# Performance work log

Hardware: AMD Instinct MI355X
Metric: run time of the kernel (lower is better)

## Reference

```python
import jax, jax.numpy as jnp
import numpy as np

CROSSOVER_MAGNITUDE = 0.3
MUTATION_FACTOR = 0.3

B, A, H = 16, 512, 8  # batch, activation_size (== dim_emb), n_head


def setup_inputs() -> dict:
    key = jax.random.key(0)
    ks = jax.random.split(key, 11)
    d = A
    s = 0.02  # small init scale for weights
    return {
        "Q": jax.random.normal(ks[0], (B, A, A), jnp.float32),
        "K": jax.random.normal(ks[1], (B, A, A), jnp.float32),
        "V": jax.random.normal(ks[2], (B, A), jnp.float32),
        "WQ_w": jax.random.normal(ks[3], (d, d), jnp.float32) * s,
        "WQ_b": jax.random.normal(ks[4], (d,), jnp.float32) * s,
        "WK_w": jax.random.normal(ks[5], (d, d), jnp.float32) * s,
        "WK_b": jax.random.normal(ks[6], (d,), jnp.float32) * s,
        "WV_w": jax.random.normal(ks[7], (d, d), jnp.float32) * s,
        "WV_b": jax.random.normal(ks[8], (d,), jnp.float32) * s,
        "WO_w": jax.random.normal(ks[9], (d, d * H), jnp.float32) * s,
        "WO_b": jax.random.normal(ks[10], (d,), jnp.float32) * s,
    }


def _attention_core(Qp, Kp, Vp, WO_w, WO_b):
    # Qp, Kp: (B, A, A) projected; identical across heads in the original
    # (heads are copies stacked before shared Linear), so compute once
    # and broadcast. Vp: (B, A).
    rkey = jax.random.key(42)
    kp, km, kr1, kr2 = jax.random.split(rkey, 4)

    am0 = jnp.einsum('bji,bjk->bik', Qp, Kp) / jnp.sqrt(jnp.float32(8.0))
    am = jnp.broadcast_to(am0[:, None], (B, H, A, A))  # (B,H,A,A)

    def mutate(a):
        # elementwise multiply by U(1-mf, 1+mf) noise
        m = jax.random.uniform(km, a.shape, jnp.float32,
                               1.0 - MUTATION_FACTOR, 1.0 + MUTATION_FACTOR)
        return a * m

    def crossover(a):
        # swap the tail segments [c:] of two random rows per (batch, head)
        c = A - int(A * CROSSOVER_MAGNITUDE)
        r1 = jax.random.randint(kr1, (B, H), 0, A)
        r2 = jax.random.randint(kr2, (B, H), 0, A)
        bi = jnp.arange(B)[:, None]
        hi = jnp.arange(H)[None, :]
        tails = a[..., c:]                     # (B,H,A,A-c)
        t1 = tails[bi, hi, r1]                 # (B,H,A-c)
        t2 = tails[bi, hi, r2]
        tails = tails.at[bi, hi, r1].set(t2).at[bi, hi, r2].set(t1)
        return jnp.concatenate([a[..., :c], tails], axis=-1)

    p = jax.random.uniform(kp, ())
    am = jax.lax.cond(p <= 0.6, mutate, crossover, am)

    attn = jax.nn.softmax(am, axis=-1)               # (B,H,A,A)
    out = jnp.einsum('bhij,bj->bhi', attn, Vp)       # attn @ V[...,None] squeezed
    out = out.reshape(B, H * A)
    return out @ WO_w.T + WO_b                       # (B, A)


def reference(Q, K, V, WQ_w, WQ_b, WK_w, WK_b, WV_w, WV_b, WO_w, WO_b):
    Qp = Q @ WQ_w.T + WQ_b   # (B,A,A), same for every head
    Kp = K @ WK_w.T + WK_b
    Vp = V @ WV_w.T + WV_b   # (B,A)
    return _attention_core(Qp, Kp, Vp, WO_w, WO_b)
```

## Files before the change

kernel.cpp:

```cpp
#include <hip/hip_runtime.h>
#include <stdint.h>
#include <string.h>

#define B_ 16
#define A_ 512
#define H_ 8
#define C_CROSS 359
#define LDSTRIDE 40

typedef short short8 __attribute__((ext_vector_type(8)));
typedef float floatx4 __attribute__((ext_vector_type(4)));

__host__ __device__ __forceinline__ uint32_t rotl32(uint32_t x, int r) {
#ifdef __HIP_DEVICE_COMPILE__
  return __builtin_amdgcn_alignbit(x, x, 32 - r);
#else
  return (x << r) | (x >> (32 - r));
#endif
}

__host__ __device__ __forceinline__ void tf2x32(uint32_t k0, uint32_t k1,
                                                uint32_t x0, uint32_t x1,
                                                uint32_t& o0, uint32_t& o1) {
  uint32_t ks2 = k0 ^ k1 ^ 0x1BD11BDAu;
  x0 += k0; x1 += k1;
#define TFR(r) { x0 += x1; x1 = rotl32(x1, r); x1 ^= x0; }
  TFR(13) TFR(15) TFR(26) TFR(6)   x0 += k1;  x1 += ks2 + 1u;
  TFR(17) TFR(29) TFR(16) TFR(24)  x0 += ks2; x1 += k0 + 2u;
  TFR(13) TFR(15) TFR(26) TFR(6)   x0 += k0;  x1 += k1 + 3u;
  TFR(17) TFR(29) TFR(16) TFR(24)  x0 += k1;  x1 += ks2 + 4u;
  TFR(13) TFR(15) TFR(26) TFR(6)   x0 += ks2; x1 += k0 + 5u;
#undef TFR
  o0 = x0; o1 = x1;
}

__host__ __device__ __forceinline__ float bits2u01(uint32_t bits) {
  uint32_t v = (bits >> 9) | 0x3f800000u;
  float f;
#ifdef __HIP_DEVICE_COMPILE__
  f = __uint_as_float(v);
#else
  memcpy(&f, &v, 4);
#endif
  return f - 1.0f;
}

__device__ __forceinline__ void tsplit(float x, short& h, short& l) {
  uint32_t u = __float_as_uint(x);
  float hf = __uint_as_float(u & 0xffff0000u);
  h = (short)(u >> 16);
  l = (short)(__float_as_uint(x - hf) >> 16);
}

__device__ __forceinline__ void tsplit8(const float4& v0, const float4& v1,
                                        short8& h, short8& l) {
  float xs[8] = {v0.x, v0.y, v0.z, v0.w, v1.x, v1.y, v1.z, v1.w};
#pragma unroll
  for (int j = 0; j < 8; ++j) {
    short hh, ll;
    tsplit(xs[j], hh, ll);
    h[j] = hh; l[j] = ll;
  }
}

__global__ __launch_bounds__(256, 2) void lin_mfma2(
    const float* __restrict__ Xq, const float* __restrict__ Wq,
    const float* __restrict__ bq, ushort* __restrict__ QptH, ushort* __restrict__ QptL,
    const float* __restrict__ Xk, const float* __restrict__ Wk,
    const float* __restrict__ bk, ushort* __restrict__ KptH, ushort* __restrict__ KptL) {
  int bid = blockIdx.x;
  int z = bid >> 8;
  int rem = bid & 255;
  int ti = rem >> 2, tn = rem & 3;
  const float* X = z ? Xk : Xq;
  const float* W = z ? Wk : Wq;
  const float* bias = z ? bk : bq;
  ushort* OH = z ? KptH : QptH;
  ushort* OL = z ? KptL : QptL;

  __shared__ __align__(16) char smem[40960];
  ushort (*Ah)[LDSTRIDE] = (ushort(*)[LDSTRIDE])(smem);
  ushort (*Al)[LDSTRIDE] = (ushort(*)[LDSTRIDE])(smem + 10240);
  ushort (*Bh)[LDSTRIDE] = (ushort(*)[LDSTRIDE])(smem + 20480);
  ushort (*Bl)[LDSTRIDE] = (ushort(*)[LDSTRIDE])(smem + 30720);
  uint32_t (*cs)[132] = (uint32_t(*)[132])(smem);

  int tid = threadIdx.x;
  int w = tid >> 6, lane = tid & 63, quad = lane >> 4, l16 = lane & 15;
  int wm = (w >> 1) * 64, wn = (w & 1) * 64;
  int m0 = ti * 128;
  int n0 = tn * 128;

  float bv[4];
#pragma unroll
  for (int nt = 0; nt < 4; ++nt) bv[nt] = bias[n0 + wn + nt * 16 + l16];

  const float* pX[2];
  const float* pW[2];
  int mW[2], kgW[2];
#pragma unroll
  for (int g = 0; g < 2; ++g) {
    int gid = g * 256 + tid;
    int m = gid >> 2, kg = gid & 3;
    mW[g] = m; kgW[g] = kg;
    pX[g] = X + (size_t)(m0 + m) * 512 + kg * 8;
    pW[g] = W + (size_t)(n0 + m) * 512 + kg * 8;
  }

  float4 ra[2][2], rb[2][2];
#pragma unroll
  for (int g = 0; g < 2; ++g) {
    ra[g][0] = *(const float4*)(pX[g]);
    ra[g][1] = *(const float4*)(pX[g] + 4);
    rb[g][0] = *(const float4*)(pW[g]);
    rb[g][1] = *(const float4*)(pW[g] + 4);
  }

  floatx4 acc[4][4] = {};

  for (int k0 = 0; k0 < 512; k0 += 32) {
    __syncthreads();
#pragma unroll
    for (int g = 0; g < 2; ++g) {
      short8 h8, l8;
      tsplit8(ra[g][0], ra[g][1], h8, l8);
      *(short8*)&Ah[mW[g]][kgW[g] * 8] = h8;
      *(short8*)&Al[mW[g]][kgW[g] * 8] = l8;
      tsplit8(rb[g][0], rb[g][1], h8, l8);
      *(short8*)&Bh[mW[g]][kgW[g] * 8] = h8;
      *(short8*)&Bl[mW[g]][kgW[g] * 8] = l8;
    }
    __syncthreads();
    if (k0 < 480) {
      int kn = k0 + 32;
#pragma unroll
      for (int g = 0; g < 2; ++g) {
        ra[g][0] = *(const float4*)(pX[g] + kn);
        ra[g][1] = *(const float4*)(pX[g] + kn + 4);
        rb[g][0] = *(const float4*)(pW[g] + kn);
        rb[g][1] = *(const float4*)(pW[g] + kn + 4);
      }
    }
    short8 fAh[4], fAl[4], fBh[4], fBl[4];
#pragma unroll
    for (int t4 = 0; t4 < 4; ++t4) {
      int ma = wm + t4 * 16 + l16;
      int nb = wn + t4 * 16 + l16;
      fAh[t4] = *(const short8*)&Ah[ma][quad * 8];
      fAl[t4] = *(const short8*)&Al[ma][quad * 8];
      fBh[t4] = *(const short8*)&Bh[nb][quad * 8];
      fBl[t4] = *(const short8*)&Bl[nb][quad * 8];
    }
#pragma unroll
    for (int mt = 0; mt < 4; ++mt)
#pragma unroll
      for (int nt = 0; nt < 4; ++nt) {
        acc[mt][nt] = __builtin_amdgcn_mfma_f32_16x16x32_bf16(fAh[mt], fBh[nt], acc[mt][nt], 0, 0, 0);
        acc[mt][nt] = __builtin_amdgcn_mfma_f32_16x16x32_bf16(fAh[mt], fBl[nt], acc[mt][nt], 0, 0, 0);
        acc[mt][nt] = __builtin_amdgcn_mfma_f32_16x16x32_bf16(fAl[mt], fBh[nt], acc[mt][nt], 0, 0, 0);
      }
  }

  __syncthreads();
  int bb = m0 >> 9, i0 = m0 & 511;
  for (int p = 0; p < 2; ++p) {
    if ((w & 1) == p) {
#pragma unroll
      for (int mt = 0; mt < 4; ++mt)
#pragma unroll
        for (int nt = 0; nt < 4; ++nt)
#pragma unroll
          for (int rr = 0; rr < 4; ++rr) {
            float val = acc[mt][nt][rr] + bv[nt];
            uint32_t u = __float_as_uint(val);
            uint32_t hi = u & 0xffff0000u;
            uint32_t lo = __float_as_uint(val - __uint_as_float(hi)) >> 16;
            cs[nt * 16 + l16][wm + mt * 16 + quad * 4 + rr] = hi | lo;
          }
    }
    __syncthreads();
    {
      int col_l = tid >> 2, iseg = (tid & 3) * 32;
      int d = n0 + p * 64 + col_l;
      size_t obase = ((size_t)(bb * 512 + d)) * 512 + i0 + iseg;
      ushort* oh = OH + obase;
      ushort* ol = OL + obase;
#pragma unroll
      for (int sgi = 0; sgi < 4; ++sgi) {
        short8 hv, lv;
#pragma unroll
        for (int j = 0; j < 8; ++j) {
          uint32_t v = cs[col_l][iseg + sgi * 8 + j];
          hv[j] = (short)(v >> 16);
          lv[j] = (short)(v & 0xffffu);
        }
        *(short8*)(oh + sgi * 8) = hv;
        *(short8*)(ol + sgi * 8) = lv;
      }
    }
    __syncthreads();
  }
}

__global__ __launch_bounds__(256, 2) void am_mfma2(
    const ushort* __restrict__ QH, const ushort* __restrict__ QL,
    const ushort* __restrict__ KH, const ushort* __restrict__ KL,
    float* __restrict__ am0) {
  int bid = blockIdx.x;
  int xcd = bid & 7, slot = bid >> 3;
  int bz = xcd + 8 * (slot >> 4);
  int tt = slot & 15, ti = tt >> 2, tk = tt & 3;
  int bm0 = ti * 128, bn0 = tk * 128;
  size_t base = (size_t)bz * 262144;

  __shared__ __align__(16) char smem[40960];
  ushort (*Ah)[LDSTRIDE] = (ushort(*)[LDSTRIDE])(smem);
  ushort (*Al)[LDSTRIDE] = (ushort(*)[LDSTRIDE])(smem + 10240);
  ushort (*Bh)[LDSTRIDE] = (ushort(*)[LDSTRIDE])(smem + 20480);
  ushort (*Bl)[LDSTRIDE] = (ushort(*)[LDSTRIDE])(smem + 30720);

  int tid = threadIdx.x;
  int w = tid >> 6, lane = tid & 63, quad = lane >> 4, l16 = lane & 15;
  int wm = (w >> 1) * 64, wn = (w & 1) * 64;

  const ushort *pAH[2], *pAL[2], *pBH[2], *pBL[2];
  int mW[2], kgW[2];
#pragma unroll
  for (int g = 0; g < 2; ++g) {
    int gid = g * 256 + tid;
    int m = gid >> 2, kg = gid & 3;
    mW[g] = m; kgW[g] = kg;
    size_t offA = base + (size_t)(bm0 + m) * 512 + kg * 8;
    size_t offB = base + (size_t)(bn0 + m) * 512 + kg * 8;
    pAH[g] = QH + offA; pAL[g] = QL + offA;
    pBH[g] = KH + offB; pBL[g] = KL + offB;
  }

  short8 rah[2], ral[2], rbh[2], rbl[2];
#pragma unroll
  for (int g = 0; g < 2; ++g) {
    rah[g] = *(const short8*)(pAH[g]);
    ral[g] = *(const short8*)(pAL[g]);
    rbh[g] = *(const short8*)(pBH[g]);
    rbl[g] = *(const short8*)(pBL[g]);
  }

  floatx4 acc[4][4] = {};

  for (int k0 = 0; k0 < 512; k0 += 32) {
    __syncthreads();
#pragma unroll
    for (int g = 0; g < 2; ++g) {
      *(short8*)&Ah[mW[g]][kgW[g] * 8] = rah[g];
      *(short8*)&Al[mW[g]][kgW[g] * 8] = ral[g];
      *(short8*)&Bh[mW[g]][kgW[g] * 8] = rbh[g];
      *(short8*)&Bl[mW[g]][kgW[g] * 8] = rbl[g];
    }
    __syncthreads();
    if (k0 < 480) {
      int kn = k0 + 32;
#pragma unroll
      for (int g = 0; g < 2; ++g) {
        rah[g] = *(const short8*)(pAH[g] + kn);
        ral[g] = *(const short8*)(pAL[g] + kn);
        rbh[g] = *(const short8*)(pBH[g] + kn);
        rbl[g] = *(const short8*)(pBL[g] + kn);
      }
    }
    short8 fAh[4], fAl[4], fBh[4], fBl[4];
#pragma unroll
    for (int t4 = 0; t4 < 4; ++t4) {
      int ma = wm + t4 * 16 + l16;
      int nb = wn + t4 * 16 + l16;
      fAh[t4] = *(const short8*)&Ah[ma][quad * 8];
      fAl[t4] = *(const short8*)&Al[ma][quad * 8];
      fBh[t4] = *(const short8*)&Bh[nb][quad * 8];
      fBl[t4] = *(const short8*)&Bl[nb][quad * 8];
    }
#pragma unroll
    for (int mt = 0; mt < 4; ++mt)
#pragma unroll
      for (int nt = 0; nt < 4; ++nt) {
        acc[mt][nt] = __builtin_amdgcn_mfma_f32_16x16x32_bf16(fAh[mt], fBh[nt], acc[mt][nt], 0, 0, 0);
        acc[mt][nt] = __builtin_amdgcn_mfma_f32_16x16x32_bf16(fAh[mt], fBl[nt], acc[mt][nt], 0, 0, 0);
        acc[mt][nt] = __builtin_amdgcn_mfma_f32_16x16x32_bf16(fAl[mt], fBh[nt], acc[mt][nt], 0, 0, 0);
      }
  }
  const float scale = 0.35355339059327373f;
#pragma unroll
  for (int mt = 0; mt < 4; ++mt)
#pragma unroll
    for (int nt = 0; nt < 4; ++nt)
#pragma unroll
      for (int rr = 0; rr < 4; ++rr) {
        int row = bm0 + wm + mt * 16 + quad * 4 + rr;
        int col = bn0 + wn + nt * 16 + l16;
        am0[((size_t)(bz * 512 + row)) * 512 + col] = acc[mt][nt][rr] * scale;
      }
}

__global__ __launch_bounds__(256) void small_gemm(
    const float* __restrict__ X, const float* __restrict__ W,
    const float* __restrict__ bias, float* __restrict__ out, int K) {
  __shared__ float xs[16 * 260];
  __shared__ float ws[16 * 260];
  int tid = threadIdx.x;
  int j0 = blockIdx.x * 16;
  int k0 = blockIdx.y * 256;
#pragma unroll
  for (int it = 0; it < 4; ++it) {
    int idx = it * 256 + tid;
    int rr = idx >> 6, kk4 = idx & 63;
    float4 xv = *(const float4*)(X + (size_t)rr * K + k0 + kk4 * 4);
    float4 wv = *(const float4*)(W + (size_t)(j0 + rr) * K + k0 + kk4 * 4);
    *(float4*)&xs[rr * 260 + kk4 * 4] = xv;
    *(float4*)&ws[rr * 260 + kk4 * 4] = wv;
  }
  __syncthreads();
  int b = tid & 15, j = tid >> 4;
  const float* xr = &xs[b * 260];
  const float* wr = &ws[j * 260];
  float acc = 0.f;
#pragma unroll
  for (int kk = 0; kk < 256; kk += 4) {
    float4 a = *(const float4*)(xr + kk);
    float4 w4 = *(const float4*)(wr + kk);
    acc += a.x * w4.x + a.y * w4.y + a.z * w4.z + a.w * w4.w;
  }
  if (blockIdx.y == 0) acc += bias[j0 + j];
  atomicAdd(&out[b * 512 + j0 + j], acc);
}

__global__ __launch_bounds__(256) void soft_mut(
    const float* __restrict__ am0, const float* __restrict__ Vp,
    float* __restrict__ oa, uint32_t km0, uint32_t km1) {
  int tid = threadIdx.x;
  int w = tid >> 6, lane = tid & 63;
  int rrow = blockIdx.x * 4 + w;
  int b = rrow >> 12, h = (rrow >> 9) & 7, i = rrow & 511;
  const float* ar = am0 + ((size_t)((b << 9) + i)) * A_ + lane;
  const float* vr = Vp + (b << 9) + lane;
  uint32_t Lb = ((((uint32_t)(((b * 8 + h) << 9) + i)) << 9)) + (uint32_t)lane;
  float s = 0.f, wsum = 0.f;
#pragma unroll
  for (int j = 0; j < 8; ++j) {
    float a = ar[64 * j];
    float vv = vr[64 * j];
    uint32_t o0, o1;
    tf2x32(km0, km1, 0u, Lb + 64u * (uint32_t)j, o0, o1);
    uint32_t bits = o0 ^ o1;
    float f = __uint_as_float((bits >> 9) | 0x3f800000u);
    float m = fmaxf(0.7f, __builtin_fmaf(f, 0.6f, 0.1f));
    float e = __expf(a * m);
    s += e;
    wsum += e * vv;
  }
#pragma unroll
  for (int o = 32; o; o >>= 1) { s += __shfl_xor(s, o); wsum += __shfl_xor(wsum, o); }
  if (lane == 0) oa[(((size_t)(b * 8 + h)) << 9) + i] = wsum / s;
}

struct CrossCfg { int r1[B_ * H_]; int r2[B_ * H_]; };

__global__ __launch_bounds__(256) void soft_cross(
    const float* __restrict__ am0, const float* __restrict__ Vp,
    float* __restrict__ oa, CrossCfg cfg) {
  int tid = threadIdx.x;
  int w = tid >> 6, lane = tid & 63;
  int rrow = blockIdx.x * 4 + w;
  int b = rrow >> 12, h = (rrow >> 9) & 7, i = rrow & 511;
  int rr1 = cfg.r1[b * 8 + h], rr2 = cfg.r2[b * 8 + h];
  int src = (i == rr2) ? rr1 : ((i == rr1) ? rr2 : i);
  const float* ar = am0 + ((size_t)((b << 9) + i)) * A_;
  const float* ar2 = am0 + ((size_t)((b << 9) + src)) * A_;
  const float* vr = Vp + (b << 9);
  float s = 0.f, wsum = 0.f;
#pragma unroll
  for (int j = 0; j < 8; ++j) {
    int k = lane + 64 * j;
    float x = (k >= C_CROSS) ? ar2[k] : ar[k];
    float e = __expf(x);
    s += e;
    wsum += e * vr[k];
  }
#pragma unroll
  for (int o = 32; o; o >>= 1) { s += __shfl_xor(s, o); wsum += __shfl_xor(wsum, o); }
  if (lane == 0) oa[(((size_t)(b * 8 + h)) << 9) + i] = wsum / s;
}

extern "C" void kernel_launch(void* const* d_in, const int* in_sizes, int n_in,
                              void* d_out, int out_size, void* d_ws, size_t ws_size,
                              hipStream_t stream) {
  (void)in_sizes; (void)n_in; (void)out_size; (void)ws_size;
  const float* Q    = (const float*)d_in[0];
  const float* K    = (const float*)d_in[1];
  const float* V    = (const float*)d_in[2];
  const float* WQ_w = (const float*)d_in[3];
  const float* WQ_b = (const float*)d_in[4];
  const float* WK_w = (const float*)d_in[5];
  const float* WK_b = (const float*)d_in[6];
  const float* WV_w = (const float*)d_in[7];
  const float* WV_b = (const float*)d_in[8];
  const float* WO_w = (const float*)d_in[9];
  const float* WO_b = (const float*)d_in[10];
  float* out = (float*)d_out;

  char* ws = (char*)d_ws;
  ushort* QptH = (ushort*)(ws);
  ushort* QptL = (ushort*)(ws + (size_t)8388608);
  ushort* KptH = (ushort*)(ws + (size_t)16777216);
  ushort* KptL = (ushort*)(ws + (size_t)25165824);
  float*  am0  = (float*) (ws + (size_t)33554432);
  float*  Vp   = (float*) (ws + (size_t)50331648);
  float*  oa   = (float*) (ws + (size_t)50331648 + 65536);

  uint32_t kp0, kp1, km0, km1, kr10, kr11, kr20, kr21, a, bbits;
  tf2x32(0u, 42u, 0u, 0u, kp0, kp1);
  tf2x32(0u, 42u, 0u, 1u, km0, km1);
  tf2x32(0u, 42u, 0u, 2u, kr10, kr11);
  tf2x32(0u, 42u, 0u, 3u, kr20, kr21);
  tf2x32(kp0, kp1, 0u, 0u, a, bbits);
  float p = bits2u01(a ^ bbits);
  if (p < 0.f) p = 0.f;
  bool mutate = (p <= 0.6f);

  hipMemsetAsync(Vp, 0, 16 * 512 * sizeof(float), stream);
  hipMemsetAsync(out, 0, 16 * 512 * sizeof(float), stream);

  lin_mfma2<<<512, 256, 0, stream>>>(Q, WQ_w, WQ_b, QptH, QptL,
                                     K, WK_w, WK_b, KptH, KptL);
  small_gemm<<<dim3(32, 2), 256, 0, stream>>>(V, WV_w, WV_b, Vp, 512);
  am_mfma2<<<256, 256, 0, stream>>>(QptH, QptL, KptH, KptL, am0);
  if (mutate) {
    soft_mut<<<16384, 256, 0, stream>>>(am0, Vp, oa, km0, km1);
  } else {
    CrossCfg cfg;
    uint32_t c0, c1;
    tf2x32(kr10, kr11, 0u, 1u, c0, c1);
    for (int t = 0; t < B_ * H_; ++t) {
      tf2x32(c0, c1, 0u, (uint32_t)t, a, bbits);
      cfg.r1[t] = (int)((a ^ bbits) & 511u);
    }
    tf2x32(kr20, kr21, 0u, 1u, c0, c1);
    for (int t = 0; t < B_ * H_; ++t) {
      tf2x32(c0, c1, 0u, (uint32_t)t, a, bbits);
      cfg.r2[t] = (int)((a ^ bbits) & 511u);
    }
    soft_cross<<<16384, 256, 0, stream>>>(am0, Vp, oa, cfg);
  }
  small_gemm<<<dim3(32, 16), 256, 0, stream>>>(oa, WO_w, WO_b, out, 4096);
}
```

Before: 223.4 us.

## Fuse score GEMM with mutated softmax-weighted reduction per head

```diff
diff --git a/kernel.cpp b/kernel.cpp
--- a/kernel.cpp
+++ b/kernel.cpp
@@ -202,6 +202,127 @@
   }
 }
 
+__global__ __launch_bounds__(512, 2) void amsoft(
+    const ushort* __restrict__ QH, const ushort* __restrict__ QL,
+    const ushort* __restrict__ KH, const ushort* __restrict__ KL,
+    const float* __restrict__ Vp,
+    float* __restrict__ oaW, float* __restrict__ oaS,
+    uint32_t km0, uint32_t km1) {
+  int bid = blockIdx.x;
+  int xcd = bid & 7, slot = bid >> 3;
+  int bz = xcd + 8 * (slot >> 4);
+  int tt = slot & 15, ti = tt >> 2, tk = tt & 3;
+  int bm0 = ti * 128, bn0 = tk * 128;
+  size_t base = (size_t)bz * 262144;
+
+  __shared__ __align__(16) char smem[40960];
+  ushort (*Ah)[LDSTRIDE] = (ushort(*)[LDSTRIDE])(smem);
+  ushort (*Al)[LDSTRIDE] = (ushort(*)[LDSTRIDE])(smem + 10240);
+  ushort (*Bh)[LDSTRIDE] = (ushort(*)[LDSTRIDE])(smem + 20480);
+  ushort (*Bl)[LDSTRIDE] = (ushort(*)[LDSTRIDE])(smem + 30720);
+
+  int tid = threadIdx.x;
+  int w = tid >> 6, lane = tid & 63, quad = lane >> 4, l16 = lane & 15;
+  int wm = (w >> 1) * 32, wn = (w & 1) * 64;
+
+  int sm = tid >> 2, skg = tid & 3;
+  size_t offA = base + (size_t)(bm0 + sm) * 512 + skg * 8;
+  size_t offB = base + (size_t)(bn0 + sm) * 512 + skg * 8;
+  const ushort* pAH = QH + offA; const ushort* pAL = QL + offA;
+  const ushort* pBH = KH + offB; const ushort* pBL = KL + offB;
+
+  short8 rah = *(const short8*)pAH, ral = *(const short8*)pAL;
+  short8 rbh = *(const short8*)pBH, rbl = *(const short8*)pBL;
+
+  floatx4 acc[2][4] = {};
+
+  for (int k0 = 0; k0 < 512; k0 += 32) {
+    __syncthreads();
+    *(short8*)&Ah[sm][skg * 8] = rah;
+    *(short8*)&Al[sm][skg * 8] = ral;
+    *(short8*)&Bh[sm][skg * 8] = rbh;
+    *(short8*)&Bl[sm][skg * 8] = rbl;
+    __syncthreads();
+    if (k0 < 480) {
+      int kn = k0 + 32;
+      rah = *(const short8*)(pAH + kn);
+      ral = *(const short8*)(pAL + kn);
+      rbh = *(const short8*)(pBH + kn);
+      rbl = *(const short8*)(pBL + kn);
+    }
+    short8 fAh[2], fAl[2], fBh[4], fBl[4];
+#pragma unroll
+    for (int mt = 0; mt < 2; ++mt) {
+      int ma = wm + mt * 16 + l16;
+      fAh[mt] = *(const short8*)&Ah[ma][quad * 8];
+      fAl[mt] = *(const short8*)&Al[ma][quad * 8];
+    }
+#pragma unroll
+    for (int nt = 0; nt < 4; ++nt) {
+      int nb = wn + nt * 16 + l16;
+      fBh[nt] = *(const short8*)&Bh[nb][quad * 8];
+      fBl[nt] = *(const short8*)&Bl[nb][quad * 8];
+    }
+#pragma unroll
+    for (int mt = 0; mt < 2; ++mt)
+#pragma unroll
+      for (int nt = 0; nt < 4; ++nt) {
+        acc[mt][nt] = __builtin_amdgcn_mfma_f32_16x16x32_bf16(fAh[mt], fBh[nt], acc[mt][nt], 0, 0, 0);
+        acc[mt][nt] = __builtin_amdgcn_mfma_f32_16x16x32_bf16(fAh[mt], fBl[nt], acc[mt][nt], 0, 0, 0);
+        acc[mt][nt] = __builtin_amdgcn_mfma_f32_16x16x32_bf16(fAl[mt], fBh[nt], acc[mt][nt], 0, 0, 0);
+      }
+  }
+
+  const float scale = 0.35355339059327373f;
+  float vv[4];
+#pragma unroll
+  for (int nt = 0; nt < 4; ++nt)
+    vv[nt] = Vp[(bz << 9) + bn0 + wn + nt * 16 + l16];
+  uint32_t Lbz = (uint32_t)bz * 2097152u;
+
+#pragma unroll
+  for (int mt = 0; mt < 2; ++mt) {
+#pragma unroll
+    for (int rr = 0; rr < 4; ++rr) {
+      int row = bm0 + wm + mt * 16 + quad * 4 + rr;
+      uint32_t Lrow = Lbz + (uint32_t)row * 512u;
+      float sh[8] = {0.f, 0.f, 0.f, 0.f, 0.f, 0.f, 0.f, 0.f};
+      float wh[8] = {0.f, 0.f, 0.f, 0.f, 0.f, 0.f, 0.f, 0.f};
+#pragma unroll
+      for (int nt = 0; nt < 4; ++nt) {
+        float a = acc[mt][nt][rr] * scale;
+        uint32_t L = Lrow + (uint32_t)(bn0 + wn + nt * 16 + l16);
+        float vn = vv[nt];
+#pragma unroll
+        for (int h = 0; h < 8; ++h) {
+          uint32_t o0, o1;
+          tf2x32(km0, km1, 0u, L + (uint32_t)h * 262144u, o0, o1);
+          uint32_t bits = o0 ^ o1;
+          float f = __uint_as_float((bits >> 9) | 0x3f800000u);
+          float m = fmaxf(0.7f, __builtin_fmaf(f, 0.6f, 0.1f));
+          float e = __expf(a * m);
+          sh[h] += e;
+          wh[h] += e * vn;
+        }
+      }
+#pragma unroll
+      for (int h = 0; h < 8; ++h) {
+        float s = sh[h], ww = wh[h];
+#pragma unroll
+        for (int o = 1; o < 16; o <<= 1) {
+          s += __shfl_xor(s, o);
+          ww += __shfl_xor(ww, o);
+        }
+        if (l16 == 0) {
+          int idx = ((bz * 8 + h) << 9) + row;
+          atomicAdd(&oaS[idx], s);
+          atomicAdd(&oaW[idx], ww);
+        }
+      }
+    }
+  }
+}
+
 __global__ __launch_bounds__(256, 2) void am_mfma2(
     const ushort* __restrict__ QH, const ushort* __restrict__ QL,
     const ushort* __restrict__ KH, const ushort* __restrict__ KL,
@@ -331,40 +452,49 @@
   atomicAdd(&out[b * 512 + j0 + j], acc);
 }
 
-__global__ __launch_bounds__(256) void soft_mut(
-    const float* __restrict__ am0, const float* __restrict__ Vp,
-    float* __restrict__ oa, uint32_t km0, uint32_t km1) {
+__global__ __launch_bounds__(256) void final_gemm(
+    const float* __restrict__ oaW, const float* __restrict__ oaS,
+    const float* __restrict__ W, const float* __restrict__ bias,
+    float* __restrict__ out) {
+  __shared__ float xs[16 * 260];
+  __shared__ float ws[16 * 260];
   int tid = threadIdx.x;
-  int w = tid >> 6, lane = tid & 63;
-  int rrow = blockIdx.x * 4 + w;
-  int b = rrow >> 12, h = (rrow >> 9) & 7, i = rrow & 511;
-  const float* ar = am0 + ((size_t)((b << 9) + i)) * A_ + lane;
-  const float* vr = Vp + (b << 9) + lane;
-  uint32_t Lb = ((((uint32_t)(((b * 8 + h) << 9) + i)) << 9)) + (uint32_t)lane;
-  float s = 0.f, wsum = 0.f;
-#pragma unroll
-  for (int j = 0; j < 8; ++j) {
-    float a = ar[64 * j];
-    float vv = vr[64 * j];
-    uint32_t o0, o1;
-    tf2x32(km0, km1, 0u, Lb + 64u * (uint32_t)j, o0, o1);
-    uint32_t bits = o0 ^ o1;
-    float f = __uint_as_float((bits >> 9) | 0x3f800000u);
-    float m = fmaxf(0.7f, __builtin_fmaf(f, 0.6f, 0.1f));
-    float e = __expf(a * m);
-    s += e;
-    wsum += e * vv;
-  }
-#pragma unroll
-  for (int o = 32; o; o >>= 1) { s += __shfl_xor(s, o); wsum += __shfl_xor(wsum, o); }
-  if (lane == 0) oa[(((size_t)(b * 8 + h)) << 9) + i] = wsum / s;
+  int j0 = blockIdx.x * 16;
+  int k0 = blockIdx.y * 256;
+#pragma unroll
+  for (int it = 0; it < 4; ++it) {
+    int idx = it * 256 + tid;
+    int rr = idx >> 6, kk4 = idx & 63;
+    size_t off = (size_t)rr * 4096 + k0 + kk4 * 4;
+    float4 nw = *(const float4*)(oaW + off);
+    float4 dn = *(const float4*)(oaS + off);
+    float4 wv = *(const float4*)(W + (size_t)(j0 + rr) * 4096 + k0 + kk4 * 4);
+    float4 xv;
+    xv.x = nw.x / dn.x; xv.y = nw.y / dn.y;
+    xv.z = nw.z / dn.z; xv.w = nw.w / dn.w;
+    *(float4*)&xs[rr * 260 + kk4 * 4] = xv;
+    *(float4*)&ws[rr * 260 + kk4 * 4] = wv;
+  }
+  __syncthreads();
+  int b = tid & 15, j = tid >> 4;
+  const float* xr = &xs[b * 260];
+  const float* wr = &ws[j * 260];
+  float acc = 0.f;
+#pragma unroll
+  for (int kk = 0; kk < 256; kk += 4) {
+    float4 a = *(const float4*)(xr + kk);
+    float4 w4 = *(const float4*)(wr + kk);
+    acc += a.x * w4.x + a.y * w4.y + a.z * w4.z + a.w * w4.w;
+  }
+  if (blockIdx.y == 0) acc += bias[j0 + j];
+  atomicAdd(&out[b * 512 + j0 + j], acc);
 }
 
 struct CrossCfg { int r1[B_ * H_]; int r2[B_ * H_]; };
 
 __global__ __launch_bounds__(256) void soft_cross(
     const float* __restrict__ am0, const float* __restrict__ Vp,
-    float* __restrict__ oa, CrossCfg cfg) {
+    float* __restrict__ oaW, float* __restrict__ oaS, CrossCfg cfg) {
   int tid = threadIdx.x;
   int w = tid >> 6, lane = tid & 63;
   int rrow = blockIdx.x * 4 + w;
@@ -385,7 +515,11 @@
   }
 #pragma unroll
   for (int o = 32; o; o >>= 1) { s += __shfl_xor(s, o); wsum += __shfl_xor(wsum, o); }
-  if (lane == 0) oa[(((size_t)(b * 8 + h)) << 9) + i] = wsum / s;
+  if (lane == 0) {
+    int idx = (((b * 8 + h)) << 9) + i;
+    oaW[idx] = wsum;
+    oaS[idx] = s;
+  }
 }
 
 extern "C" void kernel_launch(void* const* d_in, const int* in_sizes, int n_in,
@@ -412,7 +546,6 @@
   ushort* KptL = (ushort*)(ws + (size_t)25165824);
   float*  am0  = (float*) (ws + (size_t)33554432);
   float*  Vp   = (float*) (ws + (size_t)50331648);
-  float*  oa   = (float*) (ws + (size_t)50331648 + 65536);
 
   uint32_t kp0, kp1, km0, km1, kr10, kr11, kr20, kr21, a, bbits;
   tf2x32(0u, 42u, 0u, 0u, kp0, kp1);
@@ -430,10 +563,16 @@
   lin_mfma2<<<512, 256, 0, stream>>>(Q, WQ_w, WQ_b, QptH, QptL,
                                      K, WK_w, WK_b, KptH, KptL);
   small_gemm<<<dim3(32, 2), 256, 0, stream>>>(V, WV_w, WV_b, Vp, 512);
-  am_mfma2<<<256, 256, 0, stream>>>(QptH, QptL, KptH, KptL, am0);
+
   if (mutate) {
-    soft_mut<<<16384, 256, 0, stream>>>(am0, Vp, oa, km0, km1);
+    float* oaW = (float*)(ws + (size_t)33554432);
+    float* oaS = (float*)(ws + (size_t)33554432 + 262144);
+    hipMemsetAsync(oaW, 0, 2 * 262144, stream);
+    amsoft<<<256, 512, 0, stream>>>(QptH, QptL, KptH, KptL, Vp, oaW, oaS, km0, km1);
+    final_gemm<<<dim3(32, 16), 256, 0, stream>>>(oaW, oaS, WO_w, WO_b, out);
   } else {
+    float* oaW = (float*)(ws + (size_t)50331648 + 65536);
+    float* oaS = (float*)(ws + (size_t)50331648 + 65536 + 262144);
     CrossCfg cfg;
     uint32_t c0, c1;
     tf2x32(kr10, kr11, 0u, 1u, c0, c1);
@@ -446,7 +585,8 @@
       tf2x32(c0, c1, 0u, (uint32_t)t, a, bbits);
       cfg.r2[t] = (int)((a ^ bbits) & 511u);
     }
-    soft_cross<<<16384, 256, 0, stream>>>(am0, Vp, oa, cfg);
-  }
-  small_gemm<<<dim3(32, 16), 256, 0, stream>>>(oa, WO_w, WO_b, out, 4096);
-}
+    am_mfma2<<<256, 256, 0, stream>>>(QptH, QptL, KptH, KptL, am0);
+    soft_cross<<<16384, 256, 0, stream>>>(am0, Vp, oaW, oaS, cfg);
+    final_gemm<<<dim3(32, 16), 256, 0, stream>>>(oaW, oaS, WO_w, WO_b, out);
+  }
+}
```

After: 297.8 us. +33.3%, slower.

## Process all heads per row in soft_mut to reuse am0 and Vp loads

Applied to the files above, without the earlier changes.

```diff
diff --git a/kernel.cpp b/kernel.cpp
--- a/kernel.cpp
+++ b/kernel.cpp
@@ -43,6 +43,12 @@
   memcpy(&f, &v, 4);
 #endif
   return f - 1.0f;
+}
+
+__device__ __forceinline__ float exp2_native(float x) {
+  float r;
+  asm("v_exp_f32 %0, %1\n\ts_nop 0" : "=v"(r) : "v"(x));
+  return r;
 }
 
 __device__ __forceinline__ void tsplit(float x, short& h, short& l) {
@@ -337,27 +343,42 @@
   int tid = threadIdx.x;
   int w = tid >> 6, lane = tid & 63;
   int rrow = blockIdx.x * 4 + w;
-  int b = rrow >> 12, h = (rrow >> 9) & 7, i = rrow & 511;
-  const float* ar = am0 + ((size_t)((b << 9) + i)) * A_ + lane;
-  const float* vr = Vp + (b << 9) + lane;
-  uint32_t Lb = ((((uint32_t)(((b * 8 + h) << 9) + i)) << 9)) + (uint32_t)lane;
-  float s = 0.f, wsum = 0.f;
-#pragma unroll
-  for (int j = 0; j < 8; ++j) {
-    float a = ar[64 * j];
-    float vv = vr[64 * j];
-    uint32_t o0, o1;
-    tf2x32(km0, km1, 0u, Lb + 64u * (uint32_t)j, o0, o1);
-    uint32_t bits = o0 ^ o1;
-    float f = __uint_as_float((bits >> 9) | 0x3f800000u);
-    float m = fmaxf(0.7f, __builtin_fmaf(f, 0.6f, 0.1f));
-    float e = __expf(a * m);
-    s += e;
-    wsum += e * vv;
-  }
-#pragma unroll
-  for (int o = 32; o; o >>= 1) { s += __shfl_xor(s, o); wsum += __shfl_xor(wsum, o); }
-  if (lane == 0) oa[(((size_t)(b * 8 + h)) << 9) + i] = wsum / s;
+  int b = rrow >> 9, i = rrow & 511;
+  int k0 = lane * 8;
+  const float* ar = am0 + (((size_t)rrow) << 9) + k0;
+  const float* vr = Vp + (b << 9) + k0;
+  float4 a0 = *(const float4*)ar, a1 = *(const float4*)(ar + 4);
+  float4 v0 = *(const float4*)vr, v1 = *(const float4*)(vr + 4);
+  const float LOG2E = 1.4426950408889634f;
+  float a2[8] = {a0.x * LOG2E, a0.y * LOG2E, a0.z * LOG2E, a0.w * LOG2E,
+                 a1.x * LOG2E, a1.y * LOG2E, a1.z * LOG2E, a1.w * LOG2E};
+  float vv[8] = {v0.x, v0.y, v0.z, v0.w, v1.x, v1.y, v1.z, v1.w};
+  uint32_t Lbase = (uint32_t)b * 2097152u + (uint32_t)i * 512u + (uint32_t)k0;
+  float outv[8];
+#pragma unroll
+  for (int h = 0; h < 8; ++h) {
+    uint32_t Lh = Lbase + (uint32_t)h * 262144u;
+    float s = 0.f, wsum = 0.f;
+#pragma unroll
+    for (int j = 0; j < 8; ++j) {
+      uint32_t o0, o1;
+      tf2x32(km0, km1, 0u, Lh + (uint32_t)j, o0, o1);
+      uint32_t bits = o0 ^ o1;
+      float f = __uint_as_float((bits >> 9) | 0x3f800000u);
+      float m = fmaxf(0.7f, __builtin_fmaf(f, 0.6f, 0.1f));
+      float e = exp2_native(a2[j] * m);
+      s += e;
+      wsum += e * vv[j];
+    }
+#pragma unroll
+    for (int o = 32; o; o >>= 1) { s += __shfl_xor(s, o); wsum += __shfl_xor(wsum, o); }
+    outv[h] = wsum / s;
+  }
+  if (lane == 0) {
+    int ob = (b << 12) + i;
+#pragma unroll
+    for (int h = 0; h < 8; ++h) oa[ob + (h << 9)] = outv[h];
+  }
 }
 
 struct CrossCfg { int r1[B_ * H_]; int r2[B_ * H_]; };
@@ -432,7 +453,7 @@
   small_gemm<<<dim3(32, 2), 256, 0, stream>>>(V, WV_w, WV_b, Vp, 512);
   am_mfma2<<<256, 256, 0, stream>>>(QptH, QptL, KptH, KptL, am0);
   if (mutate) {
-    soft_mut<<<16384, 256, 0, stream>>>(am0, Vp, oa, km0, km1);
+    soft_mut<<<2048, 256, 0, stream>>>(am0, Vp, oa, km0, km1);
   } else {
     CrossCfg cfg;
     uint32_t c0, c1;
```

Result: no change. 222.7 us (-0.3%).
